# Performance work log

Measured on AMD Instinct MI355X. Metric: run time of the kernel, lower is better.

The kernel has to match this reference:

```python
import jax, jax.numpy as jnp
import numpy as np

B, S, H, NH, K = 8, 1024, 1024, 16, 512
HD = H // NH  # head dim = 64


def setup_inputs() -> dict:
    key = jax.random.key(0)
    ks = jax.random.split(key, 9)
    hidden_states = jax.random.normal(ks[0], (B, S, H), jnp.float32)
    # remain_layers: exactly K nonzero entries per row (static max_tokens = K)
    scores = jax.random.uniform(ks[1], (B, S))
    thresh = jnp.sort(scores, axis=1)[:, S - K][:, None]
    remain_layers = (scores >= thresh).astype(jnp.int32)
    attention_mask = jnp.zeros((B, 1, 1, S), jnp.float32)  # additive mask
    init = 0.02
    Wq = jax.random.normal(ks[2], (H, H), jnp.float32) * init
    bq = jnp.zeros((H,), jnp.float32)
    Wk = jax.random.normal(ks[3], (H, H), jnp.float32) * init
    bk = jnp.zeros((H,), jnp.float32)
    Wv = jax.random.normal(ks[4], (H, H), jnp.float32) * init
    bv = jnp.zeros((H,), jnp.float32)
    return {"hidden_states": hidden_states, "attention_mask": attention_mask,
            "remain_layers": remain_layers, "Wq": Wq, "bq": bq,
            "Wk": Wk, "bk": bk, "Wv": Wv, "bv": bv}


def _heads(x):  # [B, L, H] -> [B, NH, L, HD]
    b, l, _ = x.shape
    return x.reshape(b, l, NH, HD).transpose(0, 2, 1, 3)


def reference(hidden_states, attention_mask, remain_layers, Wq, bq, Wk, bk, Wv, bv):
    # get_reduced_hidden: per-row gather of tokens with remain_layers > 0,
    # in original position order, zero-padded to max_tokens (= K here).
    order = jnp.argsort(1 - remain_layers, axis=1, stable=True)  # nonzeros first, order kept
    idx = order[:, :K]                                           # [B, K]
    reduced = jnp.take_along_axis(hidden_states, idx[:, :, None], axis=1)  # [B, K, H]
    valid = (jnp.take_along_axis(remain_layers, idx, axis=1) > 0)
    reduced = reduced * valid[:, :, None].astype(reduced.dtype)  # zero-pad slots

    q = _heads(reduced @ Wq.T + bq)          # [B, NH, K, HD]
    k = _heads(hidden_states @ Wk.T + bk)    # [B, NH, S, HD]
    v = _heads(hidden_states @ Wv.T + bv)    # [B, NH, S, HD]

    scores = jnp.einsum('bhqd,bhkd->bhqk', q, k) / np.sqrt(HD).astype(np.float32)
    scores = scores + attention_mask         # additive mask broadcast
    probs = jax.nn.softmax(scores, axis=-1)  # dropout is identity at eval
    ctx = jnp.einsum('bhqk,bhkd->bhqd', probs, v)  # [B, NH, K, HD]
    ctx = ctx.transpose(0, 2, 1, 3).reshape(B, K, H)
    return ctx
```

## Files before the change

kernel.cpp:

```cpp
#include <hip/hip_runtime.h>
#include <hip/hip_bf16.h>
#include <stdint.h>

#define S_LEN 1024
#define HDIM  1024
#define NHEADS 16
#define HEAD_D 64
#define KSEL  512
#define BATCH 8

typedef unsigned short ushort_t;
typedef __attribute__((ext_vector_type(8))) __bf16 bf16x8;
typedef __attribute__((ext_vector_type(4))) float  f32x4;
typedef __attribute__((ext_vector_type(16))) float f32x16;

typedef const __attribute__((address_space(1))) void cg_void;
typedef __attribute__((address_space(3))) void lds_void;

__device__ __forceinline__ void gl_lds16(const void* g, void* l) {
    __builtin_amdgcn_global_load_lds((cg_void*)g, (lds_void*)l, 16, 0, 0);
}

__device__ __forceinline__ ushort_t f2bf(float f) {
    union { float f; unsigned int i; } x; x.f = f;
    unsigned int r = (x.i + 0x7fffu + ((x.i >> 16) & 1u)) >> 16;
    return (ushort_t)r;
}

__global__ __launch_bounds__(1024) void prep_kernel(
    const float* __restrict__ hidden, const float* __restrict__ wq,
    const float* __restrict__ wk, const float* __restrict__ wv,
    const int* __restrict__ remain,
    ushort_t* __restrict__ hbf, ushort_t* __restrict__ wqb,
    ushort_t* __restrict__ wkb, ushort_t* __restrict__ wvb,
    int* __restrict__ idx, int* __restrict__ valid) {
    __shared__ int wsum[16];
    __shared__ int woff[17];
    int blk = blockIdx.x;
    if (blk < 2816) {
        const float* s; ushort_t* d; int base;
        if (blk < 2048)      { s = hidden; d = hbf; base = blk; }
        else if (blk < 2304) { s = wq; d = wqb; base = blk - 2048; }
        else if (blk < 2560) { s = wk; d = wkb; base = blk - 2304; }
        else                 { s = wv; d = wvb; base = blk - 2560; }
        int i = base * 1024 + threadIdx.x;
        float4 v = ((const float4*)s)[i];
        ushort4 o;
        o.x = f2bf(v.x); o.y = f2bf(v.y); o.z = f2bf(v.z); o.w = f2bf(v.w);
        ((ushort4*)d)[i] = o;
    } else {
        int b = blk - 2816, t = threadIdx.x;
        int r = remain[b * S_LEN + t];
        unsigned long long m = __ballot(r != 0);
        int lane = t & 63, w = t >> 6;
        int pre = __popcll(m & ((1ull << lane) - 1ull));
        if (lane == 0) wsum[w] = __popcll(m);
        __syncthreads();
        if (t == 0) { int a = 0; for (int i = 0; i < 16; i++) { woff[i] = a; a += wsum[i]; } woff[16] = a; }
        __syncthreads();
        int tot = woff[16];
        int onesBefore = woff[w] + pre;
        int slot = r ? onesBefore : (tot + (t - onesBefore));
        if (slot < KSEL) { idx[b * KSEL + slot] = t; valid[b * KSEL + slot] = r; }
    }
}

#define QSCALE 0.1803368801111244f
#define LT_PITCH 136
__global__ __launch_bounds__(256, 4) void gemm_fused(
    const ushort_t* __restrict__ hbf, const ushort_t* __restrict__ wkv,
    const ushort_t* __restrict__ wq,
    const float* __restrict__ bk, const float* __restrict__ bv,
    const float* __restrict__ bq,
    const int* __restrict__ idx, const int* __restrict__ valid,
    ushort_t* __restrict__ kp, ushort_t* __restrict__ vt, ushort_t* __restrict__ qp) {
    __shared__ __align__(16) ushort_t pool[16384];
    ushort_t* As = pool;
    ushort_t* Bs = pool + 8192;
    const int i = blockIdx.x;
    int z, bmI, bnI;
    if (i < 256) { z = 1; bmI = i >> 3; bnI = i & 7; }
    else         { z = 0; int ii = i - 256; int x = ii & 7, j = ii >> 3;
                   bmI = x * 8 + (j >> 4); bnI = j & 15; }
    const long bm = (long)bmI * 128;
    const int bn = bnI * 128;

    const int tid = threadIdx.x;
    const int lane = tid & 63;
    const int w = tid >> 6;
    const int quad = lane >> 4;
    const int cl = lane & 15;
    const int srow = w * 16 + (lane >> 2);
    const int fs = ((lane >> 2) & 3) ^ ((lane >> 4) & 3);
    const int scol = ((lane & 3) ^ fs) * 8;
    const int lds_off = w * 512 + lane * 8;
    const int wr = (w >> 1) * 64, wc = (w & 1) * 64;
    const int fr = (cl & 3) ^ ((cl >> 2) & 3);
    const int qo = (quad ^ fr) * 8;

    const ushort_t* W = z ? wq : wkv;

    long ab[2];
#pragma unroll
    for (int p = 0; p < 2; p++) {
        long gr = bm + p * 64 + srow;
        if (z == 0) ab[p] = gr * HDIM;
        else {
            int b_ = (int)(gr >> 9);
            int src = idx[(b_ << 9) + ((int)gr & 511)];
            ab[p] = ((long)(b_ << 10) + src) * HDIM;
        }
    }

    f32x4 acc[4][4] = {};

    for (int k0 = 0; k0 < HDIM; k0 += 64) {
#pragma unroll
        for (int p = 0; p < 2; p++)
#pragma unroll
            for (int hh = 0; hh < 2; hh++) {
                gl_lds16(hbf + ab[p] + k0 + hh * 32 + scol, &As[hh * 4096 + p * 2048 + lds_off]);
                gl_lds16(W + ((long)(bn + p * 64 + srow)) * HDIM + k0 + hh * 32 + scol,
                         &Bs[hh * 4096 + p * 2048 + lds_off]);
            }
        __syncthreads();
#pragma unroll
        for (int hh = 0; hh < 2; hh++) {
            bf16x8 af[4], bfr[4];
#pragma unroll
            for (int mt = 0; mt < 4; mt++)
                af[mt] = *(const bf16x8*)&As[hh * 4096 + (wr + mt * 16 + cl) * 32 + qo];
#pragma unroll
            for (int nt = 0; nt < 4; nt++)
                bfr[nt] = *(const bf16x8*)&Bs[hh * 4096 + (wc + nt * 16 + cl) * 32 + qo];
#pragma unroll
            for (int mt = 0; mt < 4; mt++)
#pragma unroll
                for (int nt = 0; nt < 4; nt++)
                    acc[mt][nt] = __builtin_amdgcn_mfma_f32_16x16x32_bf16(af[mt], bfr[nt], acc[mt][nt], 0, 0, 0);
        }
        __syncthreads();
    }

    if (z == 1) {
#pragma unroll
        for (int nt = 0; nt < 4; nt++) {
            int col = bn + wc + nt * 16 + cl;
            float bvq = bq[col];
#pragma unroll
            for (int mt = 0; mt < 4; mt++) {
                long row = bm + wr + mt * 16 + quad * 4;
#pragma unroll
                for (int r = 0; r < 4; r++) {
                    float vm = (float)valid[row + r];
                    qp[(row + r) * HDIM + col] = f2bf((acc[mt][nt][r] * vm + bvq) * QSCALE);
                }
            }
        }
    } else if (bn < 1024) {
#pragma unroll
        for (int nt = 0; nt < 4; nt++) {
            int col = bn + wc + nt * 16 + cl;
            float bvk = bk[col];
#pragma unroll
            for (int mt = 0; mt < 4; mt++) {
                long row = bm + wr + mt * 16 + quad * 4;
#pragma unroll
                for (int r = 0; r < 4; r++)
                    kp[(row + r) * HDIM + col] = f2bf(acc[mt][nt][r] + bvk);
            }
        }
    } else {
        ushort_t* Lt = pool;
        long b_ = bm >> 10, s0 = bm & 1023;
#pragma unroll
        for (int p2 = 0; p2 < 2; p2++) {
            if ((w & 1) == p2) {
#pragma unroll
                for (int nt = 0; nt < 4; nt++) {
                    int cloc = nt * 16 + cl;
                    float bvv = bv[bn - 1024 + p2 * 64 + cloc];
#pragma unroll
                    for (int mt = 0; mt < 4; mt++) {
                        int row0 = wr + mt * 16 + quad * 4;
#pragma unroll
                        for (int r = 0; r < 4; r++)
                            Lt[cloc * LT_PITCH + row0 + r] = f2bf(acc[mt][nt][r] + bvv);
                    }
                }
            }
            __syncthreads();
            int c2 = tid >> 2, quarter = tid & 3;
            long gbase = ((b_ << 10) + (bn - 1024) + p2 * 64 + c2) * 1024 + s0 + quarter * 32;
            const ushort_t* src = Lt + c2 * LT_PITCH + quarter * 32;
#pragma unroll
            for (int q8 = 0; q8 < 4; q8++)
                *(bf16x8*)(vt + gbase + q8 * 8) = *(const bf16x8*)(src + q8 * 8);
            __syncthreads();
        }
    }
}

__global__ __launch_bounds__(256, 2) void attn_kernel(
    const ushort_t* __restrict__ qp, const ushort_t* __restrict__ kp,
    const ushort_t* __restrict__ vt, const float* __restrict__ mask,
    float* __restrict__ out) {
    __shared__ __align__(16) ushort_t ks[2][4096];
    __shared__ __align__(16) ushort_t vs[2][4096];
    __shared__ float mlds[1024];
    const int tid = threadIdx.x;
    const int lane = tid & 63;
    const int w = tid >> 6;
    const int ql = lane & 31;
    const int hi = lane >> 5;
    const int qt = blockIdx.x, h = blockIdx.y, b = blockIdx.z;

    const int sr2 = tid >> 3;
    const int scS = ((tid & 7) ^ (sr2 & 7)) * 8;
    const int dOf = tid * 8;

    const long kbase = (long)b * S_LEN;
    const long vbase = (long)b * 1024 + h * HEAD_D;

    {
        float4 mv4 = *(const float4*)(mask + b * S_LEN + tid * 4);
        mlds[tid * 4 + 0] = mv4.x * 1.44269504f;
        mlds[tid * 4 + 1] = mv4.y * 1.44269504f;
        mlds[tid * 4 + 2] = mv4.z * 1.44269504f;
        mlds[tid * 4 + 3] = mv4.w * 1.44269504f;
    }

    const long qrow0 = (long)b * KSEL + qt * 128 + w * 32;
    bf16x8 aq[4];
#pragma unroll
    for (int kd = 0; kd < 4; kd++)
        aq[kd] = *(const bf16x8*)(qp + (qrow0 + ql) * HDIM + h * HEAD_D + kd * 16 + hi * 8);

    f32x16 O[2] = {};
    float l_loc = 0.f;

#pragma unroll
    for (int j = 0; j < 2; j++) {
        gl_lds16(kp + (kbase + j * 32 + sr2) * (long)HDIM + h * HEAD_D + scS, &ks[0][j * 2048 + dOf]);
        gl_lds16(vt + (vbase + j * 32 + sr2) * (long)S_LEN + scS, &vs[0][j * 2048 + dOf]);
    }

    for (int c = 0; c < S_LEN / 64; c++) {
        __asm__ volatile("s_waitcnt vmcnt(0)" ::: "memory");
        __syncthreads();
        if (c + 1 < S_LEN / 64) {
            int nb = (c + 1) & 1;
#pragma unroll
            for (int j = 0; j < 2; j++) {
                gl_lds16(kp + (kbase + (c + 1) * 64 + j * 32 + sr2) * (long)HDIM + h * HEAD_D + scS,
                         &ks[nb][j * 2048 + dOf]);
                gl_lds16(vt + (vbase + j * 32 + sr2) * (long)S_LEN + (c + 1) * 64 + scS,
                         &vs[nb][j * 2048 + dOf]);
            }
        }
        const ushort_t* kb_ = ks[c & 1];
        const ushort_t* vb_ = vs[c & 1];

        f32x16 sc[2] = {};
        __builtin_amdgcn_s_setprio(1);
#pragma unroll
        for (int kd = 0; kd < 4; kd++)
#pragma unroll
            for (int mtk = 0; mtk < 2; mtk++) {
                int row = mtk * 32 + ql;
                bf16x8 af = *(const bf16x8*)&kb_[row * 64 + (((kd * 2 + hi) ^ (row & 7)) * 8)];
                sc[mtk] = __builtin_amdgcn_mfma_f32_32x32x16_bf16(af, aq[kd], sc[mtk], 0, 0, 0);
            }
        __builtin_amdgcn_s_setprio(0);

#pragma unroll
        for (int mtk = 0; mtk < 2; mtk++)
#pragma unroll
            for (int g = 0; g < 4; g++) {
                f32x4 m4 = *(const f32x4*)&mlds[c * 64 + mtk * 32 + g * 8 + hi * 4];
#pragma unroll
                for (int j = 0; j < 4; j++) {
                    float p_ = __builtin_amdgcn_exp2f(sc[mtk][g * 4 + j] + m4[j]);
                    sc[mtk][g * 4 + j] = p_;
                    l_loc += p_;
                }
            }

        bf16x8 pa[4];
#pragma unroll
        for (int mtk = 0; mtk < 2; mtk++)
#pragma unroll
            for (int sub = 0; sub < 2; sub++) {
                unsigned a0, a1, b0, b1;
                __asm__("v_cvt_pk_bf16_f32 %0, %1, %2" : "=v"(a0)
                        : "v"(sc[mtk][sub * 8 + 0]), "v"(sc[mtk][sub * 8 + 1]));
                __asm__("v_cvt_pk_bf16_f32 %0, %1, %2" : "=v"(a1)
                        : "v"(sc[mtk][sub * 8 + 2]), "v"(sc[mtk][sub * 8 + 3]));
                __asm__("v_cvt_pk_bf16_f32 %0, %1, %2" : "=v"(b0)
                        : "v"(sc[mtk][sub * 8 + 4]), "v"(sc[mtk][sub * 8 + 5]));
                __asm__("v_cvt_pk_bf16_f32 %0, %1, %2" : "=v"(b1)
                        : "v"(sc[mtk][sub * 8 + 6]), "v"(sc[mtk][sub * 8 + 7]));
                __asm__("v_permlane32_swap_b32 %0, %1" : "+v"(a0), "+v"(b0));
                __asm__("v_permlane32_swap_b32 %0, %1" : "+v"(a1), "+v"(b1));
                union { unsigned u[4]; bf16x8 v; } fr;
                fr.u[0] = a0; fr.u[1] = a1; fr.u[2] = b0; fr.u[3] = b1;
                pa[mtk * 2 + sub] = fr.v;
            }

        __builtin_amdgcn_s_setprio(1);
#pragma unroll
        for (int ks_ = 0; ks_ < 4; ks_++)
#pragma unroll
            for (int ntd = 0; ntd < 2; ntd++) {
                int row = ntd * 32 + ql;
                bf16x8 bvf = *(const bf16x8*)&vb_[row * 64 + (((ks_ * 2 + hi) ^ (row & 7)) * 8)];
                O[ntd] = __builtin_amdgcn_mfma_f32_32x32x16_bf16(bvf, pa[ks_], O[ntd], 0, 0, 0);
            }
        __builtin_amdgcn_s_setprio(0);
    }

    l_loc += __shfl_xor(l_loc, 32, 64);

#pragma unroll
    for (int ntd = 0; ntd < 2; ntd++)
#pragma unroll
        for (int g = 0; g < 4; g++) {
            float4 o4;
            o4.x = O[ntd][g * 4 + 0] / l_loc;
            o4.y = O[ntd][g * 4 + 1] / l_loc;
            o4.z = O[ntd][g * 4 + 2] / l_loc;
            o4.w = O[ntd][g * 4 + 3] / l_loc;
            *(float4*)(out + (qrow0 + ql) * HDIM + h * HEAD_D + ntd * 32 + g * 8 + hi * 4) = o4;
        }
}

extern "C" void kernel_launch(void* const* d_in, const int* in_sizes, int n_in,
                              void* d_out, int out_size, void* d_ws, size_t ws_size,
                              hipStream_t stream) {
    const float* hidden = (const float*)d_in[0];
    const float* mask   = (const float*)d_in[1];
    const int*   remain = (const int*)d_in[2];
    const float* Wq = (const float*)d_in[3];
    const float* bq = (const float*)d_in[4];
    const float* Wk = (const float*)d_in[5];
    const float* bk = (const float*)d_in[6];
    const float* Wv = (const float*)d_in[7];
    const float* bv = (const float*)d_in[8];
    float* out = (float*)d_out;

    char* ws = (char*)d_ws;
    size_t off = 0;
    int* idx   = (int*)(ws + off); off += 16384;
    int* valid = (int*)(ws + off); off += 16384;
    ushort_t* hbf = (ushort_t*)(ws + off); off += (size_t)BATCH * S_LEN * HDIM * 2;
    ushort_t* wqb = (ushort_t*)(ws + off); off += (size_t)HDIM * HDIM * 2;
    ushort_t* wkb = (ushort_t*)(ws + off); off += (size_t)HDIM * HDIM * 2;
    ushort_t* wvb = (ushort_t*)(ws + off); off += (size_t)HDIM * HDIM * 2;
    ushort_t* qp  = (ushort_t*)(ws + off); off += (size_t)BATCH * KSEL * HDIM * 2;
    ushort_t* kp  = (ushort_t*)(ws + off); off += (size_t)BATCH * S_LEN * HDIM * 2;
    ushort_t* vt  = (ushort_t*)(ws + off); off += (size_t)BATCH * S_LEN * HDIM * 2;

    prep_kernel<<<2824, 1024, 0, stream>>>(hidden, Wq, Wk, Wv, remain,
                                           hbf, wqb, wkb, wvb, idx, valid);
    gemm_fused<<<1280, 256, 0, stream>>>(hbf, wkb, wqb, bk, bv, bq,
                                         idx, valid, kp, vt, qp);
    attn_kernel<<<dim3(4, NHEADS, BATCH), 256, 0, stream>>>(qp, kp, vt, mask, out);
}
```

Measured before the change: 190.4 us.

## Triple-buffer K/V tiles in attention with prefetch depth two and partial vmcnt waits

The attention kernel moves from double to triple buffering of its K and V LDS tiles, issuing loads two chunks ahead. It waits with partial vmcnt counts so the next tile's loads can stay in flight while the current tile is computed. This should hide more global-load latency, at the cost of extra LDS per block, which may reduce occupancy. The GEMM block-index mapping is also reordered to change the tile traversal order, which affects cache locality.

```diff
diff --git a/kernel.cpp b/kernel.cpp
--- a/kernel.cpp
+++ b/kernel.cpp
@@ -26,6 +26,10 @@
     unsigned int r = (x.i + 0x7fffu + ((x.i >> 16) & 1u)) >> 16;
     return (ushort_t)r;
 }
+
+#define BAR() __asm__ volatile("s_barrier" ::: "memory")
+#define VMCNT(n) __asm__ volatile("s_waitcnt vmcnt(" #n ")" ::: "memory")
+#define LGKM0() __asm__ volatile("s_waitcnt lgkmcnt(0)" ::: "memory")
 
 __global__ __launch_bounds__(1024) void prep_kernel(
     const float* __restrict__ hidden, const float* __restrict__ wq,
@@ -81,7 +85,7 @@
     int z, bmI, bnI;
     if (i < 256) { z = 1; bmI = i >> 3; bnI = i & 7; }
     else         { z = 0; int ii = i - 256; int x = ii & 7, j = ii >> 3;
-                   bmI = x * 8 + (j >> 4); bnI = j & 15; }
+                   bmI = x * 8 + (j & 7); bnI = j >> 3; }
     const long bm = (long)bmI * 128;
     const int bn = bnI * 128;
 
@@ -205,8 +209,8 @@
     const ushort_t* __restrict__ qp, const ushort_t* __restrict__ kp,
     const ushort_t* __restrict__ vt, const float* __restrict__ mask,
     float* __restrict__ out) {
-    __shared__ __align__(16) ushort_t ks[2][4096];
-    __shared__ __align__(16) ushort_t vs[2][4096];
+    __shared__ __align__(16) ushort_t ks[3][4096];
+    __shared__ __align__(16) ushort_t vs[3][4096];
     __shared__ float mlds[1024];
     const int tid = threadIdx.x;
     const int lane = tid & 63;
@@ -239,27 +243,31 @@
     f32x16 O[2] = {};
     float l_loc = 0.f;
 
-#pragma unroll
-    for (int j = 0; j < 2; j++) {
-        gl_lds16(kp + (kbase + j * 32 + sr2) * (long)HDIM + h * HEAD_D + scS, &ks[0][j * 2048 + dOf]);
-        gl_lds16(vt + (vbase + j * 32 + sr2) * (long)S_LEN + scS, &vs[0][j * 2048 + dOf]);
-    }
-
+    auto stage = [&](int t, int slot) {
+#pragma unroll
+        for (int j = 0; j < 2; j++) {
+            gl_lds16(kp + (kbase + t * 64 + j * 32 + sr2) * (long)HDIM + h * HEAD_D + scS,
+                     &ks[slot][j * 2048 + dOf]);
+            gl_lds16(vt + (vbase + j * 32 + sr2) * (long)S_LEN + t * 64 + scS,
+                     &vs[slot][j * 2048 + dOf]);
+        }
+    };
+
+    stage(0, 0);
+    stage(1, 1);
+    LGKM0();
+
+    int slotC = 0;
+    int slotP = 2;
     for (int c = 0; c < S_LEN / 64; c++) {
-        __asm__ volatile("s_waitcnt vmcnt(0)" ::: "memory");
-        __syncthreads();
-        if (c + 1 < S_LEN / 64) {
-            int nb = (c + 1) & 1;
-#pragma unroll
-            for (int j = 0; j < 2; j++) {
-                gl_lds16(kp + (kbase + (c + 1) * 64 + j * 32 + sr2) * (long)HDIM + h * HEAD_D + scS,
-                         &ks[nb][j * 2048 + dOf]);
-                gl_lds16(vt + (vbase + j * 32 + sr2) * (long)S_LEN + (c + 1) * 64 + scS,
-                         &vs[nb][j * 2048 + dOf]);
-            }
-        }
-        const ushort_t* kb_ = ks[c & 1];
-        const ushort_t* vb_ = vs[c & 1];
+        BAR();
+        if (c + 2 < S_LEN / 64) stage(c + 2, slotP);
+        if (c < 14)       { VMCNT(8); }
+        else if (c == 14) { VMCNT(4); }
+        else              { VMCNT(0); }
+        BAR();
+        const ushort_t* kb_ = ks[slotC];
+        const ushort_t* vb_ = vs[slotC];
 
         f32x16 sc[2] = {};
         __builtin_amdgcn_s_setprio(1);
@@ -317,6 +325,9 @@
                 O[ntd] = __builtin_amdgcn_mfma_f32_32x32x16_bf16(bvf, pa[ks_], O[ntd], 0, 0, 0);
             }
         __builtin_amdgcn_s_setprio(0);
+
+        slotC = (slotC == 2) ? 0 : slotC + 1;
+        slotP = (slotP == 2) ? 0 : slotP + 1;
     }
 
     l_loc += __shfl_xor(l_loc, 32, 64);
```

Result: no change. 187.1 us (-1.8%).
